# Performance work log

Hardware: AMD Instinct MI355X
Metric: run time of the kernel (lower is better)

## Reference

```python
import jax, jax.numpy as jnp
import numpy as np

B, C_FEAT, C_CODE, H, W = 32, 768, 70, 28, 28
FS = 11
NEG = 5
POS_INTRA_SHIFT = 0.18
POS_INTER_SHIFT = 0.12
NEG_INTER_SHIFT = 0.46


def _norm(t):
    # F.normalize(t, dim=1, eps=1e-10)
    n = jnp.sqrt(jnp.sum(t * t, axis=1, keepdims=True))
    return t / jnp.maximum(n, 1e-10)


def _grid_sample(t, coords):
    # torch: F.grid_sample(t, coords.permute(0,2,1,3), padding_mode='border', align_corners=True)
    grid = jnp.transpose(coords, (0, 2, 1, 3))  # [N, Hg, Wg, 2], last dim = (x, y)
    N, C, Hi, Wi = t.shape
    # align_corners=True unnormalize, then border-clip the continuous coordinate
    x = jnp.clip((grid[..., 0] + 1.0) * 0.5 * (Wi - 1), 0.0, Wi - 1.0)
    y = jnp.clip((grid[..., 1] + 1.0) * 0.5 * (Hi - 1), 0.0, Hi - 1.0)
    x0 = jnp.floor(x)
    y0 = jnp.floor(y)
    wx = (x - x0)[:, None]  # broadcast over channel dim
    wy = (y - y0)[:, None]
    x0i = x0.astype(jnp.int32)
    y0i = y0.astype(jnp.int32)
    x1i = jnp.minimum(x0i + 1, Wi - 1)
    y1i = jnp.minimum(y0i + 1, Hi - 1)
    gather = jax.vmap(lambda img, yi, xi: img[:, yi, xi])  # [C,Hg,Wg] per batch elem
    v00 = gather(t, y0i, x0i)
    v01 = gather(t, y0i, x1i)
    v10 = gather(t, y1i, x0i)
    v11 = gather(t, y1i, x1i)
    return (v00 * (1.0 - wx) * (1.0 - wy) + v01 * wx * (1.0 - wy)
            + v10 * (1.0 - wx) * wy + v11 * wx * wy)


def _helper(f1, f2, c1, c2, shift):
    # fd under torch.no_grad -> stop_gradient
    fd = jnp.einsum('nchw,ncij->nhwij', _norm(f1), _norm(f2))
    old_mean = fd.mean()  # pointwise=True branch
    fd = fd - fd.mean(axis=(3, 4), keepdims=True)
    fd = jax.lax.stop_gradient(fd - fd.mean() + old_mean)
    cd = jnp.einsum('nchw,ncij->nhwij', _norm(c1), _norm(c2))
    # zero_clamp=True -> min_val=0.0; stabalize=True -> clamp max 0.8
    loss = -jnp.clip(cd, 0.0, 0.8) * (fd - shift)
    return loss, cd


def _forward(orig_feats, orig_feats_pos, orig_code, orig_code_pos,
             depth_aug_feats, depth_aug_feats_pos, coords1, coords2, perms):
    c1 = coords1 * 2.0 - 1.0
    c2 = coords2 * 2.0 - 1.0
    feats = _grid_sample(orig_feats, c1)
    code = _grid_sample(orig_code, c1)
    feats_pos = _grid_sample(orig_feats_pos, c2)
    code_pos = _grid_sample(orig_code_pos, c2)
    daf = _grid_sample(depth_aug_feats, c1)
    _ = _grid_sample(depth_aug_feats_pos, c2)  # computed (as in torch) but unused

    pos_intra_loss, pos_intra_cd = _helper(daf, daf, code, code, POS_INTRA_SHIFT)
    pos_inter_loss, pos_inter_cd = _helper(feats, feats_pos, code, code_pos, POS_INTER_SHIFT)

    neg_losses, neg_cds = [], []
    for i in range(perms.shape[0]):  # fixed small neg_samples loop
        p = perms[i]
        feats_neg = _grid_sample(orig_feats[p], c2)
        code_neg = _grid_sample(orig_code[p], c2)
        l, cd = _helper(feats, feats_neg, code, code_neg, NEG_INTER_SHIFT)
        neg_losses.append(l)
        neg_cds.append(cd)
    neg_inter_loss = jnp.concatenate(neg_losses, axis=0)
    neg_inter_cd = jnp.concatenate(neg_cds, axis=0)
    return (pos_intra_loss.mean(), pos_intra_cd,
            pos_inter_loss.mean(), pos_inter_cd,
            neg_inter_loss, neg_inter_cd)


def setup_inputs() -> dict:
    key = jax.random.key(0)
    ks = jax.random.split(key, 10)
    rng = np.random.default_rng(0)
    perms = []
    for _ in range(NEG):  # super_perm: derangement-ish permutation
        p = rng.permutation(B)
        p = np.where(p == np.arange(B), p + 1, p) % B
        perms.append(p)
    return {
        'orig_feats': jax.random.normal(ks[0], (B, C_FEAT, H, W), jnp.float32),
        'orig_feats_pos': jax.random.normal(ks[1], (B, C_FEAT, H, W), jnp.float32),
        'orig_salience': jnp.zeros((B, H, W), jnp.float32),
        'orig_salience_pos': jnp.zeros((B, H, W), jnp.float32),
        'orig_code': jax.random.normal(ks[2], (B, C_CODE, H, W), jnp.float32),
        'orig_code_pos': jax.random.normal(ks[3], (B, C_CODE, H, W), jnp.float32),
        'depth_aug_feats': jax.random.normal(ks[4], (B, C_FEAT, H, W), jnp.float32),
        'depth_aug_feats_pos': jax.random.normal(ks[5], (B, C_FEAT, H, W), jnp.float32),
        'coords1': jax.random.uniform(ks[6], (B, FS, FS, 2), jnp.float32),
        'coords2': jax.random.uniform(ks[7], (B, FS, FS, 2), jnp.float32),
        'perms': jnp.asarray(np.stack(perms), dtype=jnp.int32),
    }


def reference(orig_feats, orig_feats_pos, orig_salience, orig_salience_pos,
              orig_code, orig_code_pos, depth_aug_feats, depth_aug_feats_pos,
              coords1, coords2, perms):
    # use_salience=False: salience tensors unused
    return _forward(orig_feats, orig_feats_pos, orig_code, orig_code_pos,
                    depth_aug_feats, depth_aug_feats_pos, coords1, coords2, perms)
```

## Files before the change

kernel.cpp:

```cpp
#include <hip/hip_runtime.h>

#define CF 768
#define CCODE 70
#define NPIX 784
#define P 121
#define NB 32
#define NTOTF 468512.0f

#define OFF_PI_SCALAR 0
#define OFF_PI_CD 1
#define OFF_PO_SCALAR 468513
#define OFF_PO_CD 468514
#define OFF_NEG_LOSS 937026
#define OFF_NEG_CD 3279586

#define WS_BSUMS 0
#define WS_ADDT 768
#define WS_NSQF 1024
#define WS_NSQC 394240
#define WS_FRAG_FLOAT 480256
#define FEAT_FRAG_SHORTS 98304
#define CODE_FRAG_SHORTS 12288
#define FEATS_TOTAL_SHORTS (8 * 32 * FEAT_FRAG_SHORTS)
#define CODE_BASE_SHORTS FEATS_TOTAL_SHORTS
#define CODE_TOTAL_SHORTS (7 * 32 * CODE_FRAG_SHORTS)
#define WS_NEED2 (WS_FRAG_FLOAT + (FEATS_TOTAL_SHORTS + CODE_TOTAL_SHORTS) / 2)

typedef __attribute__((ext_vector_type(8))) short short8;
typedef __attribute__((ext_vector_type(4))) float f32x4;
typedef unsigned short ushort_t;
typedef unsigned int uint_t;

struct __attribute__((packed, aligned(4))) f2u {
  float x, y;
};

__device__ __forceinline__ float samp4(const float* __restrict__ img, int c,
                                       const int4 o, const float4 w) {
  const float* p = img + c * NPIX;
  return w.x * p[o.x] + w.y * p[o.y] + w.z * p[o.z] + w.w * p[o.w];
}

__device__ __forceinline__ void mkcoord(const float* cp, int4* o, float4* w) {
  float x = fminf(fmaxf(cp[0] * 27.f, 0.f), 27.f);
  float y = fminf(fmaxf(cp[1] * 27.f, 0.f), 27.f);
  float x0f = floorf(x), y0f = floorf(y);
  int x0 = (int)x0f, y0 = (int)y0f;
  int x1 = min(x0 + 1, 27), y1 = min(y0 + 1, 27);
  float wx = x - x0f, wy = y - y0f;
  *o = make_int4(y0 * 28 + x0, y0 * 28 + x1, y1 * 28 + x0, y1 * 28 + x1);
  *w = make_float4((1.f - wx) * (1.f - wy), wx * (1.f - wy),
                   (1.f - wx) * wy, wx * wy);
}

__device__ __forceinline__ void mkcoord2(const float* cp, int2* o, float4* w) {
  float x = fminf(fmaxf(cp[0] * 27.f, 0.f), 27.f);
  float y = fminf(fmaxf(cp[1] * 27.f, 0.f), 27.f);
  float x0f = floorf(x), y0f = floorf(y);
  int x0 = (int)x0f, y0 = (int)y0f;
  int y1 = min(y0 + 1, 27);
  float wx = x - x0f, wy = y - y0f;
  bool sh = (x0 >= 27);
  int xb = sh ? 26 : x0;
  float wa0 = sh ? 0.f : (1.f - wx) * (1.f - wy);
  float wa1 = sh ? (1.f - wy) : wx * (1.f - wy);
  float wb0 = sh ? 0.f : (1.f - wx) * wy;
  float wb1 = sh ? wy : wx * wy;
  *o = make_int2(y0 * 28 + xb, y1 * 28 + xb);
  *w = make_float4(wa0, wa1, wb0, wb1);
}

__device__ __forceinline__ ushort_t f2bf(float x) {
  uint_t u = __float_as_uint(x);
  u += 0x7fffu + ((u >> 16) & 1u);
  return (ushort_t)(u >> 16);
}

__global__ __launch_bounds__(256) void presample5(
    const float* __restrict__ OF, const float* __restrict__ OFP,
    const float* __restrict__ OC, const float* __restrict__ OCP,
    const float* __restrict__ DAF,
    const float* __restrict__ CO1, const float* __restrict__ CO2,
    const int* __restrict__ PERMS, float* __restrict__ ws) {
  ushort_t* frags = (ushort_t*)(ws + WS_FRAG_FLOAT);
  __shared__ float ssum[2][128];
  const int job = blockIdx.x, tid = threadIdx.x;
  const int pt = tid & 127, h = tid >> 7;
  const float* src;
  const float* cb;
  int slot, sub, n, octet0, niter, nch;
  size_t fragbase;
  float* nsqp;
  if (job < 3072) {
    slot = job / 384;
    int rem = job - slot * 384;
    n = rem / 12;
    sub = rem - n * 12;
    octet0 = sub * 8;
    niter = 4;
    nch = CF;
    int m = n;
    if (slot == 0) { src = DAF; cb = CO1; }
    else if (slot == 1) { src = OF; cb = CO1; }
    else if (slot == 2) { src = OFP; cb = CO2; }
    else { m = PERMS[(slot - 3) * NB + n]; src = OF; cb = CO2; }
    src += (size_t)m * CF * NPIX;
    fragbase = (size_t)(slot * 32 + n) * FEAT_FRAG_SHORTS;
    nsqp = ws + WS_NSQF + (size_t)((slot * 32 + n) * 12 + sub) * 128;
  } else {
    int q = job - 3072;
    slot = q / 96;
    int rem = q - slot * 96;
    n = rem / 3;
    sub = rem - n * 3;
    octet0 = sub * 4;
    niter = 2;
    nch = CCODE;
    int m = n;
    if (slot == 0) { src = OC; cb = CO1; }
    else if (slot == 1) { src = OCP; cb = CO2; }
    else { m = PERMS[(slot - 2) * NB + n]; src = OC; cb = CO2; }
    src += (size_t)m * CCODE * NPIX;
    fragbase = CODE_BASE_SHORTS + (size_t)(slot * 32 + n) * CODE_FRAG_SHORTS;
    nsqp = ws + WS_NSQC + (size_t)((slot * 32 + n) * 3 + sub) * 128;
  }

  int2 o2 = make_int2(0, 0);
  float4 w4 = make_float4(0.f, 0.f, 0.f, 0.f);
  if (pt < P) {
    int gi = pt / 11, gj = pt - gi * 11;
    mkcoord2(cb + (((n * 11 + gj) * 11 + gi) << 1), &o2, &w4);
  }
  const int tile = pt >> 4;
  float sumsq = 0.f;

  for (int k = 0; k < niter; ++k) {
    const int o = octet0 + 2 * k + h;
    const int c0 = o * 8;
    const float* base = src + (size_t)c0 * NPIX;
    float v[8];
    if (c0 + 7 < nch) {
      f2u pa[8], pb[8];
#pragma unroll
      for (int i = 0; i < 8; ++i) {
        const float* p = base + i * NPIX;
        pa[i] = *(const f2u*)(p + o2.x);
        pb[i] = *(const f2u*)(p + o2.y);
      }
#pragma unroll
      for (int i = 0; i < 8; ++i) {
        float x = w4.x * pa[i].x + w4.y * pa[i].y + w4.z * pb[i].x + w4.w * pb[i].y;
        v[i] = x;
        sumsq = fmaf(x, x, sumsq);
      }
    } else {
#pragma unroll
      for (int i = 0; i < 8; ++i) {
        float x = 0.f;
        if (c0 + i < nch) {
          const float* p = base + i * NPIX;
          f2u a = *(const f2u*)(p + o2.x);
          f2u b = *(const f2u*)(p + o2.y);
          x = w4.x * a.x + w4.y * a.y + w4.z * b.x + w4.w * b.y;
        }
        v[i] = x;
        sumsq = fmaf(x, x, sumsq);
      }
    }
    uint4 q;
    q.x = (uint_t)f2bf(v[0]) | ((uint_t)f2bf(v[1]) << 16);
    q.y = (uint_t)f2bf(v[2]) | ((uint_t)f2bf(v[3]) << 16);
    q.z = (uint_t)f2bf(v[4]) | ((uint_t)f2bf(v[5]) << 16);
    q.w = (uint_t)f2bf(v[6]) | ((uint_t)f2bf(v[7]) << 16);
    const int kp = o >> 2, lg = o & 3;
    const int lane = lg * 16 + (pt & 15);
    *(uint4*)(frags + fragbase + ((size_t)((kp * 8 + tile) * 64 + lane) << 3)) = q;
  }

  ssum[h][pt] = sumsq;
  __syncthreads();
  if (tid < 128) nsqp[tid] = ssum[0][tid] + ssum[1][tid];
}

__global__ __launch_bounds__(256) void gram_mfma(float* __restrict__ ws,
                                                 float* __restrict__ out) {
  const ushort_t* frags = (const ushort_t*)(ws + WS_FRAG_FLOAT);
  const int bid = blockIdx.x, pair = bid >> 5, n = bid & 31;
  const int tid = threadIdx.x, wave = tid >> 6, lane = tid & 63;
  __shared__ float invAf[128], invBf[128], invAc[128], invBc[128];
  __shared__ float red[4][3];
  const int afslot = (pair == 0) ? 0 : 1;
  const int bfslot = (pair == 0) ? 0 : (pair == 1 ? 2 : 3 + (pair - 2));
  const int bcslot = (pair == 0) ? 0 : (pair == 1 ? 1 : 2 + (pair - 2));
  if (tid < 128) {
    float s;
    const float* pf;
    pf = ws + WS_NSQF + (size_t)(afslot * 32 + n) * 12 * 128 + tid;
    s = 0.f;
#pragma unroll
    for (int u = 0; u < 12; ++u) s += pf[u * 128];
    invAf[tid] = 1.f / fmaxf(sqrtf(s), 1e-10f);
    pf = ws + WS_NSQF + (size_t)(bfslot * 32 + n) * 12 * 128 + tid;
    s = 0.f;
#pragma unroll
    for (int u = 0; u < 12; ++u) s += pf[u * 128];
    invBf[tid] = 1.f / fmaxf(sqrtf(s), 1e-10f);
    pf = ws + WS_NSQC + (size_t)(0 * 32 + n) * 3 * 128 + tid;
    s = pf[0] + pf[128] + pf[256];
    invAc[tid] = 1.f / fmaxf(sqrtf(s), 1e-10f);
    pf = ws + WS_NSQC + (size_t)(bcslot * 32 + n) * 3 * 128 + tid;
    s = pf[0] + pf[128] + pf[256];
    invBc[tid] = 1.f / fmaxf(sqrtf(s), 1e-10f);
  }
  __syncthreads();

  const short8* Af = (const short8*)(frags + (size_t)(afslot * 32 + n) * FEAT_FRAG_SHORTS);
  const short8* Bf = (const short8*)(frags + (size_t)(bfslot * 32 + n) * FEAT_FRAG_SHORTS);

  f32x4 acc[2][8];
#pragma unroll
  for (int j = 0; j < 2; ++j)
#pragma unroll
    for (int t = 0; t < 8; ++t) acc[j][t] = (f32x4){0.f, 0.f, 0.f, 0.f};

#pragma unroll 2
  for (int kp = 0; kp < 24; ++kp) {
    short8 a0 = Af[(kp * 8 + 2 * wave) * 64 + lane];
    short8 a1 = Af[(kp * 8 + 2 * wave + 1) * 64 + lane];
    short8 bv[8];
#pragma unroll
    for (int t = 0; t < 8; ++t) bv[t] = Bf[(kp * 8 + t) * 64 + lane];
#pragma unroll
    for (int t = 0; t < 8; ++t) {
      acc[0][t] = __builtin_amdgcn_mfma_f32_16x16x32_bf16(a0, bv[t], acc[0][t], 0, 0, 0);
      acc[1][t] = __builtin_amdgcn_mfma_f32_16x16x32_bf16(a1, bv[t], acc[1][t], 0, 0, 0);
    }
  }

  const int lane4 = (lane >> 4) << 2;
  const int cl15 = lane & 15;
  float sfd = 0.f;
#pragma unroll
  for (int j = 0; j < 2; ++j) {
    const int rb = (2 * wave + j) * 16 + lane4;
    const float ivr0 = invAf[rb], ivr1 = invAf[rb + 1], ivr2 = invAf[rb + 2],
                ivr3 = invAf[rb + 3];
    float rs0 = 0.f, rs1 = 0.f, rs2 = 0.f, rs3 = 0.f;
#pragma unroll
    for (int t = 0; t < 8; ++t) {
      const float ivc = invBf[t * 16 + cl15];
      float v0 = acc[j][t].x * ivr0 * ivc;
      float v1 = acc[j][t].y * ivr1 * ivc;
      float v2 = acc[j][t].z * ivr2 * ivc;
      float v3 = acc[j][t].w * ivr3 * ivc;
      acc[j][t].x = v0; acc[j][t].y = v1; acc[j][t].z = v2; acc[j][t].w = v3;
      rs0 += v0; rs1 += v1; rs2 += v2; rs3 += v3;
    }
    sfd += rs0 + rs1 + rs2 + rs3;
    rs0 += __shfl_xor(rs0, 1); rs0 += __shfl_xor(rs0, 2);
    rs0 += __shfl_xor(rs0, 4); rs0 += __shfl_xor(rs0, 8);
    rs1 += __shfl_xor(rs1, 1); rs1 += __shfl_xor(rs1, 2);
    rs1 += __shfl_xor(rs1, 4); rs1 += __shfl_xor(rs1, 8);
    rs2 += __shfl_xor(rs2, 1); rs2 += __shfl_xor(rs2, 2);
    rs2 += __shfl_xor(rs2, 4); rs2 += __shfl_xor(rs2, 8);
    rs3 += __shfl_xor(rs3, 1); rs3 += __shfl_xor(rs3, 2);
    rs3 += __shfl_xor(rs3, 4); rs3 += __shfl_xor(rs3, 8);
    const float rm0 = rs0 * (1.f / 121.f), rm1 = rs1 * (1.f / 121.f);
    const float rm2 = rs2 * (1.f / 121.f), rm3 = rs3 * (1.f / 121.f);
#pragma unroll
    for (int t = 0; t < 8; ++t) {
      acc[j][t].x -= rm0; acc[j][t].y -= rm1; acc[j][t].z -= rm2; acc[j][t].w -= rm3;
    }
  }

  int cd_base, loss_base = 0;
  if (pair == 0) cd_base = OFF_PI_CD + n * 14641;
  else if (pair == 1) cd_base = OFF_PO_CD + n * 14641;
  else {
    int t0 = ((pair - 2) * NB + n) * 14641;
    cd_base = OFF_NEG_CD + t0;
    loss_base = OFF_NEG_LOSS + t0;
  }

  if (pair >= 2) {
#pragma unroll
    for (int j = 0; j < 2; ++j) {
      const int rb = (2 * wave + j) * 16 + lane4;
      if (rb < P) {
#pragma unroll
        for (int t = 0; t < 8; ++t) {
          const int c = t * 16 + cl15;
          if (c < P) {
            float* o = out + loss_base + rb * P + c;
            o[0] = acc[j][t].x;
            if (rb + 1 < P) o[P] = acc[j][t].y;
            if (rb + 2 < P) o[2 * P] = acc[j][t].z;
            if (rb + 3 < P) o[3 * P] = acc[j][t].w;
          }
        }
      }
    }
  }

  const short8* Ac = (const short8*)(frags + CODE_BASE_SHORTS + (size_t)n * CODE_FRAG_SHORTS);
  const short8* Bc = (const short8*)(frags + CODE_BASE_SHORTS + (size_t)(bcslot * 32 + n) * CODE_FRAG_SHORTS);
  f32x4 cacc[2][8];
#pragma unroll
  for (int j = 0; j < 2; ++j)
#pragma unroll
    for (int t = 0; t < 8; ++t) cacc[j][t] = (f32x4){0.f, 0.f, 0.f, 0.f};
#pragma unroll
  for (int kp = 0; kp < 3; ++kp) {
    short8 a0 = Ac[(kp * 8 + 2 * wave) * 64 + lane];
    short8 a1 = Ac[(kp * 8 + 2 * wave + 1) * 64 + lane];
    short8 bv[8];
#pragma unroll
    for (int t = 0; t < 8; ++t) bv[t] = Bc[(kp * 8 + t) * 64 + lane];
#pragma unroll
    for (int t = 0; t < 8; ++t) {
      cacc[0][t] = __builtin_amdgcn_mfma_f32_16x16x32_bf16(a0, bv[t], cacc[0][t], 0, 0, 0);
      cacc[1][t] = __builtin_amdgcn_mfma_f32_16x16x32_bf16(a1, bv[t], cacc[1][t], 0, 0, 0);
    }
  }

  float s1 = 0.f, s2 = 0.f;
#pragma unroll
  for (int j = 0; j < 2; ++j) {
    const int rb = (2 * wave + j) * 16 + lane4;
    const float ivr0 = invAc[rb], ivr1 = invAc[rb + 1], ivr2 = invAc[rb + 2],
                ivr3 = invAc[rb + 3];
#pragma unroll
    for (int t = 0; t < 8; ++t) {
      const int c = t * 16 + cl15;
      const float ivc = invBc[c];
      float c0v = cacc[j][t].x * ivr0 * ivc;
      float c1v = cacc[j][t].y * ivr1 * ivc;
      float c2v = cacc[j][t].z * ivr2 * ivc;
      float c3v = cacc[j][t].w * ivr3 * ivc;
      if (c < P && rb < P) {
        float* o = out + cd_base + rb * P + c;
        o[0] = c0v;
        if (rb + 1 < P) o[P] = c1v;
        if (rb + 2 < P) o[2 * P] = c2v;
        if (rb + 3 < P) o[3 * P] = c3v;
      }
      if (pair < 2) {
        float cl0 = fminf(fmaxf(c0v, 0.f), 0.8f);
        float cl1 = fminf(fmaxf(c1v, 0.f), 0.8f);
        float cl2 = fminf(fmaxf(c2v, 0.f), 0.8f);
        float cl3 = fminf(fmaxf(c3v, 0.f), 0.8f);
        s1 = fmaf(cl0, acc[j][t].x, s1);
        s1 = fmaf(cl1, acc[j][t].y, s1);
        s1 = fmaf(cl2, acc[j][t].z, s1);
        s1 = fmaf(cl3, acc[j][t].w, s1);
        s2 += cl0 + cl1 + cl2 + cl3;
      }
    }
  }

#pragma unroll
  for (int m = 1; m < 64; m <<= 1) {
    sfd += __shfl_xor(sfd, m);
    s1 += __shfl_xor(s1, m);
    s2 += __shfl_xor(s2, m);
  }
  if ((tid & 63) == 0) { red[wave][0] = sfd; red[wave][1] = s1; red[wave][2] = s2; }
  __syncthreads();
  if (tid == 0) {
    float a = 0.f, b2 = 0.f, c2 = 0.f;
    for (int w = 0; w < 4; ++w) { a += red[w][0]; b2 += red[w][1]; c2 += red[w][2]; }
    float* bsums = ws + WS_BSUMS;
    bsums[bid * 3 + 0] = a;
    bsums[bid * 3 + 1] = b2;
    bsums[bid * 3 + 2] = c2;
  }
}

__global__ void loss_finish2(float* __restrict__ ws, float* __restrict__ out) {
  __shared__ float s[7][3];
  const float* bsums = ws + WS_BSUMS;
  float* addterm = ws + WS_ADDT;
  int tid = threadIdx.x;
  if (tid < 21) {
    int pr = tid / 3, k = tid % 3;
    float a = 0.f;
    for (int i = 0; i < 32; ++i) a += bsums[(pr * 32 + i) * 3 + k];
    s[pr][k] = a;
  }
  __syncthreads();
  if (tid == 0) {
    const float invN = 1.f / NTOTF;
    out[OFF_PI_SCALAR] = -(s[0][1] + (s[0][0] * invN - 0.18f) * s[0][2]) * invN;
    out[OFF_PO_SCALAR] = -(s[1][1] + (s[1][0] * invN - 0.12f) * s[1][2]) * invN;
  }
  if (tid >= 1 && tid < 6) addterm[tid - 1] = s[tid + 1][0] / NTOTF - 0.46f;
}

__global__ __launch_bounds__(256) void neg_loss_kernel(
    float* __restrict__ lossr, const float* __restrict__ cdr,
    const float* __restrict__ addterm) {
  __shared__ float at[5];
  if (threadIdx.x < 5) at[threadIdx.x] = addterm[threadIdx.x];
  __syncthreads();
  const int total4 = 5 * 117128;
  float4* l4 = (float4*)lossr;
  const float4* c4 = (const float4*)cdr;
  for (int e = blockIdx.x * 256 + threadIdx.x; e < total4; e += gridDim.x * 256) {
    int k = e / 117128;
    float4 cd = c4[e];
    float4 fv = l4[e];
    float a = at[k];
    float4 r;
    r.x = -fminf(fmaxf(cd.x, 0.f), 0.8f) * (fv.x + a);
    r.y = -fminf(fmaxf(cd.y, 0.f), 0.8f) * (fv.y + a);
    r.z = -fminf(fmaxf(cd.z, 0.f), 0.8f) * (fv.z + a);
    r.w = -fminf(fmaxf(cd.w, 0.f), 0.8f) * (fv.w + a);
    l4[e] = r;
  }
}


__global__ __launch_bounds__(256) void loss_main_fb(
    const float* __restrict__ OF, const float* __restrict__ OFP,
    const float* __restrict__ OC, const float* __restrict__ OCP,
    const float* __restrict__ DAF,
    const float* __restrict__ CO1, const float* __restrict__ CO2,
    const int* __restrict__ PERMS,
    float* __restrict__ out, float* __restrict__ bsums) {
  const int b = blockIdx.x;
  const int pair = b >> 7;
  const int rem = b & 127;
  const int n = rem >> 2;
  const int rg = rem & 3;
  const int row_start = rg * 31;
  const int rcount = min(31, P - row_start);
  const int tid = threadIdx.x;
  const int tx = tid & 15, ty = tid >> 4;

  const float *F1, *F2, *C1, *C2, *CB;
  if (pair == 0) {
    F1 = DAF + (size_t)n * CF * NPIX; F2 = F1;
    C1 = OC + (size_t)n * CCODE * NPIX; C2 = C1;
    CB = CO1;
  } else if (pair == 1) {
    F1 = OF + (size_t)n * CF * NPIX; F2 = OFP + (size_t)n * CF * NPIX;
    C1 = OC + (size_t)n * CCODE * NPIX; C2 = OCP + (size_t)n * CCODE * NPIX;
    CB = CO2;
  } else {
    int n2 = PERMS[(pair - 2) * NB + n];
    F1 = OF + (size_t)n * CF * NPIX; F2 = OF + (size_t)n2 * CF * NPIX;
    C1 = OC + (size_t)n * CCODE * NPIX; C2 = OC + (size_t)n2 * CCODE * NPIX;
    CB = CO2;
  }

  __shared__ int4 Bo[P];
  __shared__ float4 Bw[P];
  __shared__ int4 Ao[32];
  __shared__ float4 Aw[32];
  __shared__ float Abuf[CCODE][32];
  __shared__ float Bbuf[CCODE][128];
  __shared__ float invA[32], invB[128];
  __shared__ float red[4][3];

  if (tid < P) {
    int gi = tid / 11, gj = tid - gi * 11;
    const float* cp = CB + (((n * 11 + gj) * 11 + gi) << 1);
    mkcoord(cp, &Bo[tid], &Bw[tid]);
  } else if (tid >= 128 && tid < 160) {
    int r = tid - 128;
    int q = row_start + r;
    if (q < P) {
      int gi = q / 11, gj = q - gi * 11;
      const float* cp = CO1 + (((n * 11 + gj) * 11 + gi) << 1);
      mkcoord(cp, &Ao[r], &Aw[r]);
    }
  }
  __syncthreads();

  float acc[2][2][4];
#pragma unroll
  for (int kr = 0; kr < 2; ++kr)
#pragma unroll
    for (int m = 0; m < 2; ++m)
#pragma unroll
      for (int u = 0; u < 4; ++u) acc[kr][m][u] = 0.f;
  float ansq = 0.f, bnsq = 0.f;

  for (int ch = 0; ch < 12; ++ch) {
    const int c0 = ch * 64;
    if (ch) __syncthreads();
    for (int e = tid; e < 64 * 128; e += 256) {
      int col = e & 127, cc = e >> 7;
      float v = 0.f;
      if (col < P) v = samp4(F2, c0 + cc, Bo[col], Bw[col]);
      Bbuf[cc][col] = v;
    }
    for (int e = tid; e < 64 * 32; e += 256) {
      int col = e & 31, cc = e >> 5;
      float v = 0.f;
      if (col < rcount) v = samp4(F1, c0 + cc, Ao[col], Aw[col]);
      Abuf[cc][col] = v;
    }
    __syncthreads();
    if (tid < 128) {
      float s = 0.f;
      for (int cc = 0; cc < 64; ++cc) { float v = Bbuf[cc][tid]; s = fmaf(v, v, s); }
      bnsq += s;
    } else if (tid < 160) {
      int r = tid - 128;
      float s = 0.f;
      for (int cc = 0; cc < 64; ++cc) { float v = Abuf[cc][r]; s = fmaf(v, v, s); }
      ansq += s;
    }
    for (int cc = 0; cc < 64; ++cc) {
      const float2 av = *(const float2*)&Abuf[cc][ty * 2];
      const float4 b0 = *(const float4*)&Bbuf[cc][tx * 4];
      const float4 b1 = *(const float4*)&Bbuf[cc][tx * 4 + 64];
      float a[2] = {av.x, av.y};
      float bb[2][4] = {{b0.x, b0.y, b0.z, b0.w}, {b1.x, b1.y, b1.z, b1.w}};
#pragma unroll
      for (int kr = 0; kr < 2; ++kr)
#pragma unroll
        for (int m = 0; m < 2; ++m)
#pragma unroll
          for (int u = 0; u < 4; ++u)
            acc[kr][m][u] = fmaf(a[kr], bb[m][u], acc[kr][m][u]);
    }
  }
  __syncthreads();
  if (tid < 128) invB[tid] = (tid < P) ? 1.f / fmaxf(sqrtf(bnsq), 1e-10f) : 0.f;
  else if (tid < 160) {
    int r = tid - 128;
    invA[r] = (r < rcount) ? 1.f / fmaxf(sqrtf(ansq), 1e-10f) : 0.f;
  }
  __syncthreads();

  float ia[2] = {invA[2 * ty], invA[2 * ty + 1]};
  float ib[2][4];
#pragma unroll
  for (int m = 0; m < 2; ++m)
#pragma unroll
    for (int u = 0; u < 4; ++u) ib[m][u] = invB[m * 64 + tx * 4 + u];

  float fdc[2][2][4];
  float sfd = 0.f;
#pragma unroll
  for (int kr = 0; kr < 2; ++kr) {
    float part = 0.f;
#pragma unroll
    for (int m = 0; m < 2; ++m)
#pragma unroll
      for (int u = 0; u < 4; ++u) {
        float v = acc[kr][m][u] * ia[kr] * ib[m][u];
        fdc[kr][m][u] = v;
        part += v;
      }
    sfd += part;
    float rs = part;
#pragma unroll
    for (int s = 1; s < 16; s <<= 1) rs += __shfl_xor(rs, s, 16);
    float rowm = rs * (1.f / 121.f);
#pragma unroll
    for (int m = 0; m < 2; ++m)
#pragma unroll
      for (int u = 0; u < 4; ++u) fdc[kr][m][u] -= rowm;
  }
  __syncthreads();

  for (int e = tid; e < CCODE * 128; e += 256) {
    int col = e & 127, cc = e >> 7;
    float v = 0.f;
    if (col < P) v = samp4(C2, cc, Bo[col], Bw[col]);
    Bbuf[cc][col] = v;
  }
  for (int e = tid; e < CCODE * 32; e += 256) {
    int col = e & 31, cc = e >> 5;
    float v = 0.f;
    if (col < rcount) v = samp4(C1, cc, Ao[col], Aw[col]);
    Abuf[cc][col] = v;
  }
  __syncthreads();
  if (tid < 128) {
    float s = 0.f;
    for (int cc = 0; cc < CCODE; ++cc) { float v = Bbuf[cc][tid]; s = fmaf(v, v, s); }
    invB[tid] = (tid < P) ? 1.f / fmaxf(sqrtf(s), 1e-10f) : 0.f;
  } else if (tid < 160) {
    int r = tid - 128;
    float s = 0.f;
    for (int cc = 0; cc < CCODE; ++cc) { float v = Abuf[cc][r]; s = fmaf(v, v, s); }
    invA[r] = (r < rcount) ? 1.f / fmaxf(sqrtf(s), 1e-10f) : 0.f;
  }
  float cacc[2][2][4];
#pragma unroll
  for (int kr = 0; kr < 2; ++kr)
#pragma unroll
    for (int m = 0; m < 2; ++m)
#pragma unroll
      for (int u = 0; u < 4; ++u) cacc[kr][m][u] = 0.f;
  for (int cc = 0; cc < CCODE; ++cc) {
    const float2 av = *(const float2*)&Abuf[cc][ty * 2];
    const float4 b0 = *(const float4*)&Bbuf[cc][tx * 4];
    const float4 b1 = *(const float4*)&Bbuf[cc][tx * 4 + 64];
    float a[2] = {av.x, av.y};
    float bb[2][4] = {{b0.x, b0.y, b0.z, b0.w}, {b1.x, b1.y, b1.z, b1.w}};
#pragma unroll
    for (int kr = 0; kr < 2; ++kr)
#pragma unroll
      for (int m = 0; m < 2; ++m)
#pragma unroll
        for (int u = 0; u < 4; ++u)
          cacc[kr][m][u] = fmaf(a[kr], bb[m][u], cacc[kr][m][u]);
  }
  __syncthreads();
  float iac[2] = {invA[2 * ty], invA[2 * ty + 1]};
  float ibc[2][4];
#pragma unroll
  for (int m = 0; m < 2; ++m)
#pragma unroll
    for (int u = 0; u < 4; ++u) ibc[m][u] = invB[m * 64 + tx * 4 + u];

  int cd_base, loss_base = 0;
  if (pair == 0) cd_base = OFF_PI_CD + n * 14641;
  else if (pair == 1) cd_base = OFF_PO_CD + n * 14641;
  else {
    int t = ((pair - 2) * NB + n) * 14641;
    cd_base = OFF_NEG_CD + t;
    loss_base = OFF_NEG_LOSS + t;
  }

  float s1 = 0.f, s2 = 0.f;
#pragma unroll
  for (int kr = 0; kr < 2; ++kr) {
    int r = 2 * ty + kr;
    if (r < rcount) {
      int rglob = row_start + r;
#pragma unroll
      for (int m = 0; m < 2; ++m)
#pragma unroll
        for (int u = 0; u < 4; ++u) {
          int c = m * 64 + tx * 4 + u;
          if (c < P) {
            float cdv = cacc[kr][m][u] * iac[kr] * ibc[m][u];
            int idx = rglob * P + c;
            out[cd_base + idx] = cdv;
            float cl = fminf(fmaxf(cdv, 0.f), 0.8f);
            float fv = fdc[kr][m][u];
            if (pair < 2) { s1 = fmaf(cl, fv, s1); s2 += cl; }
            else out[loss_base + idx] = fv;
          }
        }
    }
  }

#pragma unroll
  for (int s = 1; s < 64; s <<= 1) {
    sfd += __shfl_xor(sfd, s);
    s1 += __shfl_xor(s1, s);
    s2 += __shfl_xor(s2, s);
  }
  int wv = tid >> 6;
  if ((tid & 63) == 0) { red[wv][0] = sfd; red[wv][1] = s1; red[wv][2] = s2; }
  __syncthreads();
  if (tid == 0) {
    float a = 0.f, bb = 0.f, cc = 0.f;
    for (int w = 0; w < 4; ++w) { a += red[w][0]; bb += red[w][1]; cc += red[w][2]; }
    bsums[b * 3 + 0] = a;
    bsums[b * 3 + 1] = bb;
    bsums[b * 3 + 2] = cc;
  }
}

__global__ void loss_finish_fb(const float* __restrict__ bsums,
                               float* __restrict__ out,
                               float* __restrict__ addterm) {
  __shared__ float s[7][3];
  int tid = threadIdx.x;
  if (tid < 21) {
    int pr = tid / 3, k = tid % 3;
    float a = 0.f;
    const float* p = bsums + (pr * 128) * 3 + k;
    for (int i = 0; i < 128; ++i) a += p[i * 3];
    s[pr][k] = a;
  }
  __syncthreads();
  if (tid == 0) {
    const float invN = 1.f / NTOTF;
    out[OFF_PI_SCALAR] = -(s[0][1] + (s[0][0] * invN - 0.18f) * s[0][2]) * invN;
    out[OFF_PO_SCALAR] = -(s[1][1] + (s[1][0] * invN - 0.12f) * s[1][2]) * invN;
  }
  if (tid >= 1 && tid < 6) addterm[tid - 1] = s[tid + 1][0] / NTOTF - 0.46f;
}

__global__ __launch_bounds__(256) void neg_loss_fb(
    float* __restrict__ lossr, const float* __restrict__ cdr,
    const float* __restrict__ addterm) {
  __shared__ float at[5];
  if (threadIdx.x < 5) at[threadIdx.x] = addterm[threadIdx.x];
  __syncthreads();
  const int total = 5 * 468512;
  for (int e = blockIdx.x * 256 + threadIdx.x; e < total; e += gridDim.x * 256) {
    int k = e / 468512;
    float cdv = cdr[e];
    float cl = fminf(fmaxf(cdv, 0.f), 0.8f);
    lossr[e] = -cl * (lossr[e] + at[k]);
  }
}

extern "C" void kernel_launch(void* const* d_in, const int* in_sizes, int n_in,
                              void* d_out, int out_size, void* d_ws,
                              size_t ws_size, hipStream_t stream) {
  const float* OF = (const float*)d_in[0];
  const float* OFP = (const float*)d_in[1];
  const float* OC = (const float*)d_in[4];
  const float* OCP = (const float*)d_in[5];
  const float* DAF = (const float*)d_in[6];
  const float* CO1 = (const float*)d_in[8];
  const float* CO2 = (const float*)d_in[9];
  const int* PERMS = (const int*)d_in[10];
  float* out = (float*)d_out;
  float* ws = (float*)d_ws;

  if (ws_size >= (size_t)WS_NEED2 * sizeof(float)) {
    hipLaunchKernelGGL(presample5, dim3(3744), dim3(256), 0, stream,
                       OF, OFP, OC, OCP, DAF, CO1, CO2, PERMS, ws);
    hipLaunchKernelGGL(gram_mfma, dim3(224), dim3(256), 0, stream, ws, out);
    hipLaunchKernelGGL(loss_finish2, dim3(1), dim3(64), 0, stream, ws, out);
    hipLaunchKernelGGL(neg_loss_kernel, dim3(1024), dim3(256), 0, stream,
                       out + OFF_NEG_LOSS, out + OFF_NEG_CD, ws + WS_ADDT);
  } else {
    float* bsums = ws;
    float* addterm = bsums + 896 * 3;
    hipLaunchKernelGGL(loss_main_fb, dim3(896), dim3(256), 0, stream,
                       OF, OFP, OC, OCP, DAF, CO1, CO2, PERMS, out, bsums);
    hipLaunchKernelGGL(loss_finish_fb, dim3(1), dim3(64), 0, stream,
                       bsums, out, addterm);
    hipLaunchKernelGGL(neg_loss_fb, dim3(2048), dim3(256), 0, stream,
                       out + OFF_NEG_LOSS, out + OFF_NEG_CD, addterm);
  }
}
```

Measured before the change: 168.9 us.

## Stage source channel planes in LDS and sample per source image, move norms to separate kernel

The presample kernel now processes each source image/channel-octet once: it streams 8 full channel planes into shared memory with coalesced float4 loads, then bilinearly samples for every consumer (including all permutation slots that reference this image) from LDS. Previously each slot did scattered global gathers from the source separately, re-reading the same image for permuted negatives. Norms are now computed in a new kernel from the bf16 fragments instead of fp32 partial sums, which adds a launch and changes norm precision to bf16-rounded values. The block count rises and every block loads full planes (784 px) even though only 121 points are sampled per slot.

New measurement: 155.5 us. 7.9% less time.

```diff
diff --git a/kernel.cpp b/kernel.cpp
--- a/kernel.cpp
+++ b/kernel.cpp
@@ -16,9 +16,9 @@
 
 #define WS_BSUMS 0
 #define WS_ADDT 768
-#define WS_NSQF 1024
-#define WS_NSQC 394240
-#define WS_FRAG_FLOAT 480256
+#define WS_INVF 1024
+#define WS_INVC 33792
+#define WS_FRAG_FLOAT 62464
 #define FEAT_FRAG_SHORTS 98304
 #define CODE_FRAG_SHORTS 12288
 #define FEATS_TOTAL_SHORTS (8 * 32 * FEAT_FRAG_SHORTS)
@@ -30,10 +30,6 @@
 typedef __attribute__((ext_vector_type(4))) float f32x4;
 typedef unsigned short ushort_t;
 typedef unsigned int uint_t;
-
-struct __attribute__((packed, aligned(4))) f2u {
-  float x, y;
-};
 
 __device__ __forceinline__ float samp4(const float* __restrict__ img, int c,
                                        const int4 o, const float4 w) {
@@ -76,110 +72,149 @@
   return (ushort_t)(u >> 16);
 }
 
-__global__ __launch_bounds__(256) void presample5(
+__device__ __forceinline__ float bflo(uint_t u) {
+  return __uint_as_float(u << 16);
+}
+__device__ __forceinline__ float bfhi(uint_t u) {
+  return __uint_as_float(u & 0xffff0000u);
+}
+
+__global__ __launch_bounds__(256) void presample_img(
     const float* __restrict__ OF, const float* __restrict__ OFP,
     const float* __restrict__ OC, const float* __restrict__ OCP,
     const float* __restrict__ DAF,
     const float* __restrict__ CO1, const float* __restrict__ CO2,
     const int* __restrict__ PERMS, float* __restrict__ ws) {
   ushort_t* frags = (ushort_t*)(ws + WS_FRAG_FLOAT);
-  __shared__ float ssum[2][128];
+  __shared__ float planes[8 * NPIX];
+  __shared__ int sh_slot[16], sh_n[16], sh_cb[16];
+  __shared__ int sh_ncs;
   const int job = blockIdx.x, tid = threadIdx.x;
-  const int pt = tid & 127, h = tid >> 7;
+
+  int tensor, m, o;
+  if (job < 3072) { tensor = 0; m = job / 96; o = job - m * 96; }
+  else if (job < 6144) { int j = job - 3072; tensor = 1; m = j / 96; o = j - m * 96; }
+  else if (job < 9216) { int j = job - 6144; tensor = 2; m = j / 96; o = j - m * 96; }
+  else if (job < 9600) { int j = job - 9216; tensor = 3; m = j / 12; o = j - m * 12; }
+  else { int j = job - 9600; tensor = 4; m = j / 12; o = j - m * 12; }
+
   const float* src;
-  const float* cb;
-  int slot, sub, n, octet0, niter, nch;
-  size_t fragbase;
-  float* nsqp;
-  if (job < 3072) {
-    slot = job / 384;
-    int rem = job - slot * 384;
-    n = rem / 12;
-    sub = rem - n * 12;
-    octet0 = sub * 8;
-    niter = 4;
-    nch = CF;
-    int m = n;
-    if (slot == 0) { src = DAF; cb = CO1; }
-    else if (slot == 1) { src = OF; cb = CO1; }
-    else if (slot == 2) { src = OFP; cb = CO2; }
-    else { m = PERMS[(slot - 3) * NB + n]; src = OF; cb = CO2; }
-    src += (size_t)m * CF * NPIX;
-    fragbase = (size_t)(slot * 32 + n) * FEAT_FRAG_SHORTS;
-    nsqp = ws + WS_NSQF + (size_t)((slot * 32 + n) * 12 + sub) * 128;
-  } else {
-    int q = job - 3072;
-    slot = q / 96;
-    int rem = q - slot * 96;
-    n = rem / 3;
-    sub = rem - n * 3;
-    octet0 = sub * 4;
-    niter = 2;
-    nch = CCODE;
-    int m = n;
-    if (slot == 0) { src = OC; cb = CO1; }
-    else if (slot == 1) { src = OCP; cb = CO2; }
-    else { m = PERMS[(slot - 2) * NB + n]; src = OC; cb = CO2; }
-    src += (size_t)m * CCODE * NPIX;
-    fragbase = CODE_BASE_SHORTS + (size_t)(slot * 32 + n) * CODE_FRAG_SHORTS;
-    nsqp = ws + WS_NSQC + (size_t)((slot * 32 + n) * 3 + sub) * 128;
-  }
-
-  int2 o2 = make_int2(0, 0);
-  float4 w4 = make_float4(0.f, 0.f, 0.f, 0.f);
-  if (pt < P) {
-    int gi = pt / 11, gj = pt - gi * 11;
-    mkcoord2(cb + (((n * 11 + gj) * 11 + gi) << 1), &o2, &w4);
-  }
-  const int tile = pt >> 4;
-  float sumsq = 0.f;
-
-  for (int k = 0; k < niter; ++k) {
-    const int o = octet0 + 2 * k + h;
-    const int c0 = o * 8;
-    const float* base = src + (size_t)c0 * NPIX;
+  int nch;
+  bool feat;
+  if (tensor == 0) { src = OF + (size_t)m * CF * NPIX; nch = CF; feat = true; }
+  else if (tensor == 1) { src = DAF + (size_t)m * CF * NPIX; nch = CF; feat = true; }
+  else if (tensor == 2) { src = OFP + (size_t)m * CF * NPIX; nch = CF; feat = true; }
+  else if (tensor == 3) { src = OC + (size_t)m * CCODE * NPIX; nch = CCODE; feat = false; }
+  else { src = OCP + (size_t)m * CCODE * NPIX; nch = CCODE; feat = false; }
+
+  if (tid == 0) {
+    int cnt = 0;
+    if (tensor == 0) {
+      sh_slot[0] = 1; sh_n[0] = m; sh_cb[0] = 0; cnt = 1;
+      for (int i = 0; i < 5; ++i)
+        for (int k = 0; k < NB; ++k)
+          if (PERMS[i * NB + k] == m) {
+            sh_slot[cnt] = 3 + i; sh_n[cnt] = k; sh_cb[cnt] = 1; ++cnt;
+          }
+    } else if (tensor == 1) { sh_slot[0] = 0; sh_n[0] = m; sh_cb[0] = 0; cnt = 1; }
+    else if (tensor == 2) { sh_slot[0] = 2; sh_n[0] = m; sh_cb[0] = 1; cnt = 1; }
+    else if (tensor == 3) {
+      sh_slot[0] = 0; sh_n[0] = m; sh_cb[0] = 0; cnt = 1;
+      for (int i = 0; i < 5; ++i)
+        for (int k = 0; k < NB; ++k)
+          if (PERMS[i * NB + k] == m) {
+            sh_slot[cnt] = 2 + i; sh_n[cnt] = k; sh_cb[cnt] = 1; ++cnt;
+          }
+    } else { sh_slot[0] = 1; sh_n[0] = m; sh_cb[0] = 1; cnt = 1; }
+    sh_ncs = cnt;
+  }
+
+  const int c0 = o * 8;
+  {
+    int valid = nch - c0;
+    valid = valid > 8 ? 8 : (valid < 0 ? 0 : valid);
+    const float* sc = src + (size_t)c0 * NPIX;
+    const int lim4 = valid * (NPIX / 4);
+    for (int e = tid; e < 8 * NPIX / 4; e += 256) {
+      float4 v = (e < lim4) ? ((const float4*)sc)[e]
+                            : make_float4(0.f, 0.f, 0.f, 0.f);
+      ((float4*)planes)[e] = v;
+    }
+  }
+  __syncthreads();
+
+  const int kp = o >> 2, lg = o & 3;
+  const int total = sh_ncs * 128;
+  for (int s = tid; s < total; s += 256) {
+    const int cs = s >> 7, pt = s & 127;
+    const int slot = sh_slot[cs], n = sh_n[cs];
+    const float* cb = sh_cb[cs] ? CO2 : CO1;
     float v[8];
-    if (c0 + 7 < nch) {
-      f2u pa[8], pb[8];
+    if (pt < P) {
+      int gi = pt / 11, gj = pt - gi * 11;
+      int2 o2;
+      float4 w4;
+      mkcoord2(cb + (((n * 11 + gj) * 11 + gi) << 1), &o2, &w4);
 #pragma unroll
       for (int i = 0; i < 8; ++i) {
-        const float* p = base + i * NPIX;
-        pa[i] = *(const f2u*)(p + o2.x);
-        pb[i] = *(const f2u*)(p + o2.y);
-      }
-#pragma unroll
-      for (int i = 0; i < 8; ++i) {
-        float x = w4.x * pa[i].x + w4.y * pa[i].y + w4.z * pb[i].x + w4.w * pb[i].y;
-        v[i] = x;
-        sumsq = fmaf(x, x, sumsq);
+        const float* pl = planes + i * NPIX;
+        v[i] = w4.x * pl[o2.x] + w4.y * pl[o2.x + 1] + w4.z * pl[o2.y] +
+               w4.w * pl[o2.y + 1];
       }
     } else {
 #pragma unroll
-      for (int i = 0; i < 8; ++i) {
-        float x = 0.f;
-        if (c0 + i < nch) {
-          const float* p = base + i * NPIX;
-          f2u a = *(const f2u*)(p + o2.x);
-          f2u b = *(const f2u*)(p + o2.y);
-          x = w4.x * a.x + w4.y * a.y + w4.z * b.x + w4.w * b.y;
-        }
-        v[i] = x;
-        sumsq = fmaf(x, x, sumsq);
-      }
+      for (int i = 0; i < 8; ++i) v[i] = 0.f;
     }
     uint4 q;
     q.x = (uint_t)f2bf(v[0]) | ((uint_t)f2bf(v[1]) << 16);
     q.y = (uint_t)f2bf(v[2]) | ((uint_t)f2bf(v[3]) << 16);
     q.z = (uint_t)f2bf(v[4]) | ((uint_t)f2bf(v[5]) << 16);
     q.w = (uint_t)f2bf(v[6]) | ((uint_t)f2bf(v[7]) << 16);
-    const int kp = o >> 2, lg = o & 3;
-    const int lane = lg * 16 + (pt & 15);
-    *(uint4*)(frags + fragbase + ((size_t)((kp * 8 + tile) * 64 + lane) << 3)) = q;
-  }
-
-  ssum[h][pt] = sumsq;
-  __syncthreads();
-  if (tid < 128) nsqp[tid] = ssum[0][tid] + ssum[1][tid];
+    size_t fragbase = feat ? (size_t)(slot * 32 + n) * FEAT_FRAG_SHORTS
+                           : CODE_BASE_SHORTS + (size_t)(slot * 32 + n) * CODE_FRAG_SHORTS;
+    *(uint4*)(frags + fragbase +
+              ((size_t)((kp * 8 + (pt >> 4)) * 64 + lg * 16 + (pt & 15)) << 3)) = q;
+  }
+}
+
+__global__ __launch_bounds__(128) void norms_kernel(float* __restrict__ ws) {
+  const ushort_t* frags = (const ushort_t*)(ws + WS_FRAG_FLOAT);
+  const int b = blockIdx.x, p = threadIdx.x;
+  float s = 0.f;
+  if (b < 256) {
+    const int slot = b >> 5, n = b & 31;
+    const uint4* F = (const uint4*)(frags + (size_t)(slot * 32 + n) * FEAT_FRAG_SHORTS);
+    for (int kp = 0; kp < 24; ++kp) {
+#pragma unroll
+      for (int lg = 0; lg < 4; ++lg) {
+        uint4 q = F[(kp * 8 + (p >> 4)) * 64 + lg * 16 + (p & 15)];
+        float a;
+        a = bflo(q.x); s = fmaf(a, a, s); a = bfhi(q.x); s = fmaf(a, a, s);
+        a = bflo(q.y); s = fmaf(a, a, s); a = bfhi(q.y); s = fmaf(a, a, s);
+        a = bflo(q.z); s = fmaf(a, a, s); a = bfhi(q.z); s = fmaf(a, a, s);
+        a = bflo(q.w); s = fmaf(a, a, s); a = bfhi(q.w); s = fmaf(a, a, s);
+      }
+    }
+    ws[WS_INVF + (slot * 32 + n) * 128 + p] = 1.f / fmaxf(sqrtf(s), 1e-10f);
+  } else {
+    const int b2 = b - 256;
+    const int slot = b2 >> 5, n = b2 & 31;
+    const uint4* F = (const uint4*)(frags + CODE_BASE_SHORTS +
+                                    (size_t)(slot * 32 + n) * CODE_FRAG_SHORTS);
+#pragma unroll
+    for (int kp = 0; kp < 3; ++kp) {
+#pragma unroll
+      for (int lg = 0; lg < 4; ++lg) {
+        uint4 q = F[(kp * 8 + (p >> 4)) * 64 + lg * 16 + (p & 15)];
+        float a;
+        a = bflo(q.x); s = fmaf(a, a, s); a = bfhi(q.x); s = fmaf(a, a, s);
+        a = bflo(q.y); s = fmaf(a, a, s); a = bfhi(q.y); s = fmaf(a, a, s);
+        a = bflo(q.z); s = fmaf(a, a, s); a = bfhi(q.z); s = fmaf(a, a, s);
+        a = bflo(q.w); s = fmaf(a, a, s); a = bfhi(q.w); s = fmaf(a, a, s);
+      }
+    }
+    ws[WS_INVC + (slot * 32 + n) * 128 + p] = 1.f / fmaxf(sqrtf(s), 1e-10f);
+  }
 }
 
 __global__ __launch_bounds__(256) void gram_mfma(float* __restrict__ ws,
@@ -193,24 +228,10 @@
   const int bfslot = (pair == 0) ? 0 : (pair == 1 ? 2 : 3 + (pair - 2));
   const int bcslot = (pair == 0) ? 0 : (pair == 1 ? 1 : 2 + (pair - 2));
   if (tid < 128) {
-    float s;
-    const float* pf;
-    pf = ws + WS_NSQF + (size_t)(afslot * 32 + n) * 12 * 128 + tid;
-    s = 0.f;
-#pragma unroll
-    for (int u = 0; u < 12; ++u) s += pf[u * 128];
-    invAf[tid] = 1.f / fmaxf(sqrtf(s), 1e-10f);
-    pf = ws + WS_NSQF + (size_t)(bfslot * 32 + n) * 12 * 128 + tid;
-    s = 0.f;
-#pragma unroll
-    for (int u = 0; u < 12; ++u) s += pf[u * 128];
-    invBf[tid] = 1.f / fmaxf(sqrtf(s), 1e-10f);
-    pf = ws + WS_NSQC + (size_t)(0 * 32 + n) * 3 * 128 + tid;
-    s = pf[0] + pf[128] + pf[256];
-    invAc[tid] = 1.f / fmaxf(sqrtf(s), 1e-10f);
-    pf = ws + WS_NSQC + (size_t)(bcslot * 32 + n) * 3 * 128 + tid;
-    s = pf[0] + pf[128] + pf[256];
-    invBc[tid] = 1.f / fmaxf(sqrtf(s), 1e-10f);
+    invAf[tid] = ws[WS_INVF + (afslot * 32 + n) * 128 + tid];
+    invBf[tid] = ws[WS_INVF + (bfslot * 32 + n) * 128 + tid];
+    invAc[tid] = ws[WS_INVC + (0 * 32 + n) * 128 + tid];
+    invBc[tid] = ws[WS_INVC + (bcslot * 32 + n) * 128 + tid];
   }
   __syncthreads();
 
@@ -721,8 +742,9 @@
   float* ws = (float*)d_ws;
 
   if (ws_size >= (size_t)WS_NEED2 * sizeof(float)) {
-    hipLaunchKernelGGL(presample5, dim3(3744), dim3(256), 0, stream,
+    hipLaunchKernelGGL(presample_img, dim3(9984), dim3(256), 0, stream,
                        OF, OFP, OC, OCP, DAF, CO1, CO2, PERMS, ws);
+    hipLaunchKernelGGL(norms_kernel, dim3(480), dim3(128), 0, stream, ws);
     hipLaunchKernelGGL(gram_mfma, dim3(224), dim3(256), 0, stream, ws, out);
     hipLaunchKernelGGL(loss_finish2, dim3(1), dim3(64), 0, stream, ws, out);
     hipLaunchKernelGGL(neg_loss_kernel, dim3(1024), dim3(256), 0, stream,
```
